# Performance work log

Measured on AMD Instinct MI355X. Metric: run time of the kernel, lower is better.

Reference implementation:

```python
import jax, jax.numpy as jnp
import numpy as np

H = 128          # image_size
FOCAL = 3.0      # camera focal length (NDC scale)
ZNEAR = 1e-2
EPS = 1e-8

def setup_inputs() -> dict:
    key = jax.random.key(0)
    k1, k2, k3, k4 = jax.random.split(key, 4)
    B, V, F = 2, 2048, 512
    verts_world = jax.random.uniform(k1, (B, V, 3), minval=-1.0, maxval=1.0, dtype=jnp.float32)
    faces = jax.random.randint(k2, (F, 3), 0, V)
    R = jnp.tile(jnp.eye(3, dtype=jnp.float32)[None], (B, 1, 1)) + 0.05 * jax.random.normal(k3, (B, 3, 3), dtype=jnp.float32)
    # camera sits 4 units back so all geometry has positive view-space depth
    T = jnp.concatenate([0.1 * jax.random.normal(k4, (B, 2), dtype=jnp.float32), jnp.full((B, 1), 4.0, jnp.float32)], axis=-1)
    return {"verts_world": verts_world, "faces": faces, "R": R, "T": T}

def _seg_d2(px, py, ax, ay, bx, by):
    # squared distance from point (px,py) to segment (a,b)
    abx, aby = bx - ax, by - ay
    apx, apy = px - ax, py - ay
    t = jnp.clip((apx * abx + apy * aby) / (abx * abx + aby * aby + EPS), 0.0, 1.0)
    dx, dy = apx - t * abx, apy - t * aby
    return dx * dx + dy * dy

def _project(verts_world, R, T):
    # world -> view (row-vector convention, as pytorch3d transform_points)
    v_view = jnp.einsum('bvj,bjk->bvk', verts_world, R) + T[:, None, :]
    z = v_view[..., 2:3]                       # view-space depth kept as screen z (as in MeshRasterizer.transform)
    xy = FOCAL * v_view[..., :2] / z           # perspective projection to NDC
    return jnp.concatenate([xy, z], axis=-1)   # [B,V,3]

def _rasterize(verts_ndc, faces):
    tri = verts_ndc[:, faces]                  # [B,F,3,3]
    def c(i, j):
        return tri[:, :, i, j][:, None, None, :]   # [B,1,1,F]
    x0, y0, z0 = c(0, 0), c(0, 1), c(0, 2)
    x1, y1, z1 = c(1, 0), c(1, 1), c(1, 2)
    x2, y2, z2 = c(2, 0), c(2, 1), c(2, 2)
    # pixel centers, pytorch3d NDC convention (+X left, +Y up)
    s = 1.0 - (2.0 * jnp.arange(H, dtype=verts_ndc.dtype) + 1.0) / H
    px = s[None, None, :, None]                # varies over W
    py = s[None, :, None, None]                # varies over H
    area = (x1 - x0) * (y2 - y0) - (y1 - y0) * (x2 - x0)      # 2 * signed area
    denom = jnp.where(jnp.abs(area) > EPS, area, EPS)
    w0 = ((x2 - x1) * (py - y1) - (y2 - y1) * (px - x1)) / denom
    w1 = ((x0 - x2) * (py - y2) - (y0 - y2) * (px - x2)) / denom
    w2 = 1.0 - w0 - w1                         # barycentrics [B,H,W,F]
    inside = (w0 >= 0) & (w1 >= 0) & (w2 >= 0)
    zp = w0 * z0 + w1 * z1 + w2 * z2           # barycentric-interpolated depth
    valid = inside & (zp > ZNEAR) & (jnp.abs(area) > EPS)
    d2 = jnp.minimum(_seg_d2(px, py, x0, y0, x1, y1),
                     jnp.minimum(_seg_d2(px, py, x1, y1, x2, y2),
                                 _seg_d2(px, py, x2, y2, x0, y0)))
    dists = jnp.where(inside, -d2, d2)         # signed squared edge distance
    zsort = jnp.where(valid, zp, jnp.inf)
    idx = jnp.argmin(zsort, axis=-1)           # nearest covering face per pixel (faces_per_pixel=1)
    hit = jnp.isfinite(jnp.min(zsort, axis=-1))
    take = lambda a: jnp.take_along_axis(a, idx[..., None], axis=-1)[..., 0]
    zbuf = jnp.where(hit, take(zp), -1.0)
    bary = jnp.stack([take(w0), take(w1), take(w2)], axis=-1)
    bary = jnp.where(hit[..., None], bary, -1.0)
    dsel = jnp.where(hit, take(dists), -1.0)
    pix_to_face = jnp.where(hit, idx, -1)
    # trailing K=1 (faces_per_pixel) dim, matching Fragments layout
    return pix_to_face[..., None], zbuf[..., None], bary[:, :, :, None, :], dsel[..., None]

def reference(verts_world, faces, R, T):
    verts_ndc = _project(verts_world, R, T)
    return _rasterize(verts_ndc, faces)
```

## Files before the change

kernel.cpp:

```cpp
#include <hip/hip_runtime.h>
#include <cstdint>

#define H_ 128
#define V_ 2048
#define F_ 512
#define B_ 2
#define FOCAL_ 3.0f
#define ZNEAR_ 0.01f
#define EPS_ 1e-8f
#define PAD_ 1e-3f

__global__ __launch_bounds__(1024) void k_prep(const float* __restrict__ vw,
                                               const int* __restrict__ faces,
                                               const float* __restrict__ R,
                                               const float* __restrict__ T,
                                               float* __restrict__ fd,
                                               float4* __restrict__ bb) {
  __shared__ float ndc[B_ * V_ * 3];
  int t = threadIdx.x;

  for (int tid = t; tid < B_ * V_; tid += 1024) {
    int b = tid >> 11;
    const float* v  = vw + tid * 3;
    const float* Rb = R + b * 9;
    const float* Tb = T + b * 3;
    float vx = v[0], vy = v[1], vz = v[2];
    float o[3];
#pragma unroll
    for (int k = 0; k < 3; ++k) {
      float a = __fadd_rn(__fadd_rn(__fmul_rn(vx, Rb[k]), __fmul_rn(vy, Rb[3 + k])),
                          __fmul_rn(vz, Rb[6 + k]));
      o[k] = __fadd_rn(a, Tb[k]);
    }
    float z = o[2];
    ndc[tid * 3 + 0] = __fdiv_rn(__fmul_rn(FOCAL_, o[0]), z);
    ndc[tid * 3 + 1] = __fdiv_rn(__fmul_rn(FOCAL_, o[1]), z);
    ndc[tid * 3 + 2] = z;
  }
  __syncthreads();

  {
    int tid = t;
    int b = tid >> 9;
    int f = tid & (F_ - 1);
    int i0 = faces[f * 3 + 0], i1 = faces[f * 3 + 1], i2 = faces[f * 3 + 2];
    const float* nb = ndc + b * V_ * 3;
    float x0 = nb[i0 * 3], y0 = nb[i0 * 3 + 1], z0 = nb[i0 * 3 + 2];
    float x1 = nb[i1 * 3], y1 = nb[i1 * 3 + 1], z1 = nb[i1 * 3 + 2];
    float x2 = nb[i2 * 3], y2 = nb[i2 * 3 + 1], z2 = nb[i2 * 3 + 2];
    float area = __fsub_rn(__fmul_rn(__fsub_rn(x1, x0), __fsub_rn(y2, y0)),
                           __fmul_rn(__fsub_rn(y1, y0), __fsub_rn(x2, x0)));
    bool ok = fabsf(area) > EPS_;
    float denom = ok ? area : EPS_;
    float* o = fd + tid * 16;
    o[0]  = x1;  o[1]  = y1;  o[2]  = x2;  o[3]  = y2;
    o[4]  = z0;  o[5]  = z1;  o[6]  = z2;  o[7]  = denom;
    o[8]  = __fsub_rn(x2, x1);  o[9]  = __fsub_rn(y2, y1);
    o[10] = __fsub_rn(x0, x2);  o[11] = __fsub_rn(y0, y2);
    o[12] = x0;  o[13] = y0;  o[14] = ok ? 1.0f : 0.0f;  o[15] = 0.0f;
    float4 box;
    if (ok) {
      box.x = fminf(fminf(x0, x1), x2) - PAD_;
      box.y = fmaxf(fmaxf(x0, x1), x2) + PAD_;
      box.z = fminf(fminf(y0, y1), y2) - PAD_;
      box.w = fmaxf(fmaxf(y0, y1), y2) + PAD_;
    } else {
      box.x = 1e30f; box.y = -1e30f; box.z = 1e30f; box.w = -1e30f;
    }
    bb[tid] = box;
  }
}

__device__ __forceinline__ float seg_d2(float px, float py, float ax, float ay,
                                        float bx, float by) {
  float abx = __fsub_rn(bx, ax), aby = __fsub_rn(by, ay);
  float apx = __fsub_rn(px, ax), apy = __fsub_rn(py, ay);
  float num = __fadd_rn(__fmul_rn(apx, abx), __fmul_rn(apy, aby));
  float den = __fadd_rn(__fadd_rn(__fmul_rn(abx, abx), __fmul_rn(aby, aby)), EPS_);
  float t = __fdiv_rn(num, den);
  t = fminf(fmaxf(t, 0.0f), 1.0f);
  float dx = __fsub_rn(apx, __fmul_rn(t, abx));
  float dy = __fsub_rn(apy, __fmul_rn(t, aby));
  return __fadd_rn(__fmul_rn(dx, dx), __fmul_rn(dy, dy));
}

__global__ __launch_bounds__(512) void k_raster(const float* __restrict__ fd,
                                                const float4* __restrict__ bb,
                                                float* __restrict__ out) {
  __shared__ float4 lf4[F_ * 4];
  __shared__ unsigned long long red[64 * 8];
  const float* lf = (const float*)lf4;
  int blk = blockIdx.x;
  int b  = blk >> 8;
  int iy = (blk >> 1) & (H_ - 1);
  int h  = blk & 1;
  int t = threadIdx.x;
  int lane = t & 63;
  int q = t >> 6;
  int ix = h * 64 + lane;

  const float4* src = (const float4*)(fd + b * F_ * 16);
  for (int i = t; i < F_ * 4; i += 512) lf4[i] = src[i];
  __syncthreads();

  float px = 1.0f - (float)(2 * ix + 1) * 0.0078125f;
  float py = 1.0f - (float)(2 * iy + 1) * 0.0078125f;
  float pxmax = 1.0f - (float)(2 * (h * 64) + 1) * 0.0078125f;
  float pxmin = 1.0f - (float)(2 * (h * 64 + 63) + 1) * 0.0078125f;

  float4 box = bb[b * F_ + q * 64 + lane];
  bool ov = (box.x <= pxmax) && (box.y >= pxmin) && (box.z <= py) && (box.w >= py);
  unsigned long long m = __ballot(ov);

  const float INF = __int_as_float(0x7f800000);
  float best = INF;
  int bidx = q * 64;

  while (m) {
    int f = q * 64 + __builtin_ctzll(m);
    m &= m - 1;
    float4 q0 = lf4[f * 4 + 0];
    float4 q1 = lf4[f * 4 + 1];
    float4 q2 = lf4[f * 4 + 2];
    float e0 = __fsub_rn(__fmul_rn(q2.x, __fsub_rn(py, q0.y)),
                         __fmul_rn(q2.y, __fsub_rn(px, q0.x)));
    float e1 = __fsub_rn(__fmul_rn(q2.z, __fsub_rn(py, q0.w)),
                         __fmul_rn(q2.w, __fsub_rn(px, q0.z)));
    bool dpos = q1.w > 0.0f;
    bool s0 = dpos ? (e0 >= 0.0f) : (e0 <= 0.0f);
    bool s1 = dpos ? (e1 >= 0.0f) : (e1 <= 0.0f);
    if (__any(s0 && s1)) {
      float w0 = __fdiv_rn(e0, q1.w);
      float w1 = __fdiv_rn(e1, q1.w);
      float w2 = __fsub_rn(__fsub_rn(1.0f, w0), w1);
      float zp = __fadd_rn(__fadd_rn(__fmul_rn(w0, q1.x), __fmul_rn(w1, q1.y)),
                           __fmul_rn(w2, q1.z));
      bool valid = s0 && s1 && (w2 >= 0.0f) && (zp > ZNEAR_);
      float zs = valid ? zp : INF;
      if (zs < best) { best = zs; bidx = f; }
    }
  }

  red[lane * 8 + q] =
      ((unsigned long long)__float_as_uint(best) << 32) | (unsigned long long)(unsigned)bidx;
  __syncthreads();

  if (q == 0) {
    unsigned long long mm = red[lane * 8];
#pragma unroll
    for (int j = 1; j < 8; ++j) {
      unsigned long long v = red[lane * 8 + j];
      mm = (v < mm) ? v : mm;
    }
    unsigned zb = (unsigned)(mm >> 32);
    int idx = (int)(mm & 0xffffffffu);
    bool hit = zb < 0x7f800000u;

    const float* Fp = &lf[idx * 16];
    float x1 = Fp[0], y1 = Fp[1], x2 = Fp[2], y2 = Fp[3];
    float z0 = Fp[4], z1 = Fp[5], z2 = Fp[6], denom = Fp[7];
    float dx21 = Fp[8], dy21 = Fp[9], dx02 = Fp[10], dy02 = Fp[11];
    float x0 = Fp[12], y0 = Fp[13];
    float w0 = __fdiv_rn(__fsub_rn(__fmul_rn(dx21, __fsub_rn(py, y1)),
                                   __fmul_rn(dy21, __fsub_rn(px, x1))), denom);
    float w1 = __fdiv_rn(__fsub_rn(__fmul_rn(dx02, __fsub_rn(py, y2)),
                                   __fmul_rn(dy02, __fsub_rn(px, x2))), denom);
    float w2 = __fsub_rn(__fsub_rn(1.0f, w0), w1);
    float zp = __fadd_rn(__fadd_rn(__fmul_rn(w0, z0), __fmul_rn(w1, z1)),
                         __fmul_rn(w2, z2));
    float d01 = seg_d2(px, py, x0, y0, x1, y1);
    float d12 = seg_d2(px, py, x1, y1, x2, y2);
    float d20 = seg_d2(px, py, x2, y2, x0, y0);
    float d2 = fminf(d01, fminf(d12, d20));

    int pix = ((b * H_ + iy) * H_) + ix;
    out[pix]                 = hit ? (float)idx : -1.0f;
    out[32768 + pix]         = hit ? zp : -1.0f;
    out[65536 + pix * 3 + 0] = hit ? w0 : -1.0f;
    out[65536 + pix * 3 + 1] = hit ? w1 : -1.0f;
    out[65536 + pix * 3 + 2] = hit ? w2 : -1.0f;
    out[163840 + pix]        = hit ? -d2 : -1.0f;
  }
}

extern "C" void kernel_launch(void* const* d_in, const int* in_sizes, int n_in,
                              void* d_out, int out_size, void* d_ws, size_t ws_size,
                              hipStream_t stream) {
  const float* vw    = (const float*)d_in[0];
  const int*   faces = (const int*)d_in[1];
  const float* R     = (const float*)d_in[2];
  const float* T     = (const float*)d_in[3];
  float* out = (float*)d_out;
  float* ws  = (float*)d_ws;
  float*  fd  = ws;
  float4* bbp = (float4*)(ws + 16384);
  k_prep<<<1, 1024, 0, stream>>>(vw, faces, R, T, fd, bbp);
  k_raster<<<512, 512, 0, stream>>>(fd, bbp, out);
}
```

Before: 84.43 us.

## Fuse projection and face setup into raster kernel, recomputing per block

Removes the single-block prep kernel and its global workspace round trip. Each of the 512 raster blocks now projects all 2048 vertices of its batch and builds the face table and bounding boxes directly in shared memory. This drops one launch and the serial single-block prep stage, at the cost of redundant per-block projection work (divisions included) and about 40 KB of shared memory per block, which may limit occupancy.

```diff
diff --git a/kernel.cpp b/kernel.cpp
--- a/kernel.cpp
+++ b/kernel.cpp
@@ -9,67 +9,6 @@
 #define ZNEAR_ 0.01f
 #define EPS_ 1e-8f
 #define PAD_ 1e-3f
-
-__global__ __launch_bounds__(1024) void k_prep(const float* __restrict__ vw,
-                                               const int* __restrict__ faces,
-                                               const float* __restrict__ R,
-                                               const float* __restrict__ T,
-                                               float* __restrict__ fd,
-                                               float4* __restrict__ bb) {
-  __shared__ float ndc[B_ * V_ * 3];
-  int t = threadIdx.x;
-
-  for (int tid = t; tid < B_ * V_; tid += 1024) {
-    int b = tid >> 11;
-    const float* v  = vw + tid * 3;
-    const float* Rb = R + b * 9;
-    const float* Tb = T + b * 3;
-    float vx = v[0], vy = v[1], vz = v[2];
-    float o[3];
-#pragma unroll
-    for (int k = 0; k < 3; ++k) {
-      float a = __fadd_rn(__fadd_rn(__fmul_rn(vx, Rb[k]), __fmul_rn(vy, Rb[3 + k])),
-                          __fmul_rn(vz, Rb[6 + k]));
-      o[k] = __fadd_rn(a, Tb[k]);
-    }
-    float z = o[2];
-    ndc[tid * 3 + 0] = __fdiv_rn(__fmul_rn(FOCAL_, o[0]), z);
-    ndc[tid * 3 + 1] = __fdiv_rn(__fmul_rn(FOCAL_, o[1]), z);
-    ndc[tid * 3 + 2] = z;
-  }
-  __syncthreads();
-
-  {
-    int tid = t;
-    int b = tid >> 9;
-    int f = tid & (F_ - 1);
-    int i0 = faces[f * 3 + 0], i1 = faces[f * 3 + 1], i2 = faces[f * 3 + 2];
-    const float* nb = ndc + b * V_ * 3;
-    float x0 = nb[i0 * 3], y0 = nb[i0 * 3 + 1], z0 = nb[i0 * 3 + 2];
-    float x1 = nb[i1 * 3], y1 = nb[i1 * 3 + 1], z1 = nb[i1 * 3 + 2];
-    float x2 = nb[i2 * 3], y2 = nb[i2 * 3 + 1], z2 = nb[i2 * 3 + 2];
-    float area = __fsub_rn(__fmul_rn(__fsub_rn(x1, x0), __fsub_rn(y2, y0)),
-                           __fmul_rn(__fsub_rn(y1, y0), __fsub_rn(x2, x0)));
-    bool ok = fabsf(area) > EPS_;
-    float denom = ok ? area : EPS_;
-    float* o = fd + tid * 16;
-    o[0]  = x1;  o[1]  = y1;  o[2]  = x2;  o[3]  = y2;
-    o[4]  = z0;  o[5]  = z1;  o[6]  = z2;  o[7]  = denom;
-    o[8]  = __fsub_rn(x2, x1);  o[9]  = __fsub_rn(y2, y1);
-    o[10] = __fsub_rn(x0, x2);  o[11] = __fsub_rn(y0, y2);
-    o[12] = x0;  o[13] = y0;  o[14] = ok ? 1.0f : 0.0f;  o[15] = 0.0f;
-    float4 box;
-    if (ok) {
-      box.x = fminf(fminf(x0, x1), x2) - PAD_;
-      box.y = fmaxf(fmaxf(x0, x1), x2) + PAD_;
-      box.z = fminf(fminf(y0, y1), y2) - PAD_;
-      box.w = fmaxf(fmaxf(y0, y1), y2) + PAD_;
-    } else {
-      box.x = 1e30f; box.y = -1e30f; box.z = 1e30f; box.w = -1e30f;
-    }
-    bb[tid] = box;
-  }
-}
 
 __device__ __forceinline__ float seg_d2(float px, float py, float ax, float ay,
                                         float bx, float by) {
@@ -84,10 +23,14 @@
   return __fadd_rn(__fmul_rn(dx, dx), __fmul_rn(dy, dy));
 }
 
-__global__ __launch_bounds__(512) void k_raster(const float* __restrict__ fd,
-                                                const float4* __restrict__ bb,
-                                                float* __restrict__ out) {
+__global__ __launch_bounds__(512) void k_all(const float* __restrict__ vw,
+                                             const int* __restrict__ faces,
+                                             const float* __restrict__ R,
+                                             const float* __restrict__ T,
+                                             float* __restrict__ out) {
+  __shared__ float ndc[V_ * 3];
   __shared__ float4 lf4[F_ * 4];
+  __shared__ float4 lbb[F_];
   __shared__ unsigned long long red[64 * 8];
   const float* lf = (const float*)lf4;
   int blk = blockIdx.x;
@@ -99,8 +42,55 @@
   int q = t >> 6;
   int ix = h * 64 + lane;
 
-  const float4* src = (const float4*)(fd + b * F_ * 16);
-  for (int i = t; i < F_ * 4; i += 512) lf4[i] = src[i];
+  {
+    const float* Rb = R + b * 9;
+    const float* Tb = T + b * 3;
+    float r00 = Rb[0], r01 = Rb[1], r02 = Rb[2];
+    float r10 = Rb[3], r11 = Rb[4], r12 = Rb[5];
+    float r20 = Rb[6], r21 = Rb[7], r22 = Rb[8];
+    float t0 = Tb[0], t1 = Tb[1], t2 = Tb[2];
+    for (int i = t; i < V_; i += 512) {
+      const float* v = vw + (b * V_ + i) * 3;
+      float vx = v[0], vy = v[1], vz = v[2];
+      float ox = __fadd_rn(__fadd_rn(__fadd_rn(__fmul_rn(vx, r00), __fmul_rn(vy, r10)),
+                                     __fmul_rn(vz, r20)), t0);
+      float oy = __fadd_rn(__fadd_rn(__fadd_rn(__fmul_rn(vx, r01), __fmul_rn(vy, r11)),
+                                     __fmul_rn(vz, r21)), t1);
+      float oz = __fadd_rn(__fadd_rn(__fadd_rn(__fmul_rn(vx, r02), __fmul_rn(vy, r12)),
+                                     __fmul_rn(vz, r22)), t2);
+      ndc[i * 3 + 0] = __fdiv_rn(__fmul_rn(FOCAL_, ox), oz);
+      ndc[i * 3 + 1] = __fdiv_rn(__fmul_rn(FOCAL_, oy), oz);
+      ndc[i * 3 + 2] = oz;
+    }
+  }
+  __syncthreads();
+
+  {
+    int f = t;
+    int i0 = faces[f * 3 + 0], i1 = faces[f * 3 + 1], i2 = faces[f * 3 + 2];
+    float x0 = ndc[i0 * 3], y0 = ndc[i0 * 3 + 1], z0 = ndc[i0 * 3 + 2];
+    float x1 = ndc[i1 * 3], y1 = ndc[i1 * 3 + 1], z1 = ndc[i1 * 3 + 2];
+    float x2 = ndc[i2 * 3], y2 = ndc[i2 * 3 + 1], z2 = ndc[i2 * 3 + 2];
+    float area = __fsub_rn(__fmul_rn(__fsub_rn(x1, x0), __fsub_rn(y2, y0)),
+                           __fmul_rn(__fsub_rn(y1, y0), __fsub_rn(x2, x0)));
+    bool ok = fabsf(area) > EPS_;
+    float denom = ok ? area : EPS_;
+    lf4[f * 4 + 0] = make_float4(x1, y1, x2, y2);
+    lf4[f * 4 + 1] = make_float4(z0, z1, z2, denom);
+    lf4[f * 4 + 2] = make_float4(__fsub_rn(x2, x1), __fsub_rn(y2, y1),
+                                 __fsub_rn(x0, x2), __fsub_rn(y0, y2));
+    lf4[f * 4 + 3] = make_float4(x0, y0, ok ? 1.0f : 0.0f, 0.0f);
+    float4 box;
+    if (ok) {
+      box.x = fminf(fminf(x0, x1), x2) - PAD_;
+      box.y = fmaxf(fmaxf(x0, x1), x2) + PAD_;
+      box.z = fminf(fminf(y0, y1), y2) - PAD_;
+      box.w = fmaxf(fmaxf(y0, y1), y2) + PAD_;
+    } else {
+      box.x = 1e30f; box.y = -1e30f; box.z = 1e30f; box.w = -1e30f;
+    }
+    lbb[f] = box;
+  }
   __syncthreads();
 
   float px = 1.0f - (float)(2 * ix + 1) * 0.0078125f;
@@ -108,7 +98,7 @@
   float pxmax = 1.0f - (float)(2 * (h * 64) + 1) * 0.0078125f;
   float pxmin = 1.0f - (float)(2 * (h * 64 + 63) + 1) * 0.0078125f;
 
-  float4 box = bb[b * F_ + q * 64 + lane];
+  float4 box = lbb[q * 64 + lane];
   bool ov = (box.x <= pxmax) && (box.y >= pxmin) && (box.z <= py) && (box.w >= py);
   unsigned long long m = __ballot(ov);
 
@@ -191,9 +181,6 @@
   const float* R     = (const float*)d_in[2];
   const float* T     = (const float*)d_in[3];
   float* out = (float*)d_out;
-  float* ws  = (float*)d_ws;
-  float*  fd  = ws;
-  float4* bbp = (float4*)(ws + 16384);
-  k_prep<<<1, 1024, 0, stream>>>(vw, faces, R, T, fd, bbp);
-  k_raster<<<512, 512, 0, stream>>>(fd, bbp, out);
+  (void)d_ws; (void)ws_size;
+  k_all<<<512, 512, 0, stream>>>(vw, faces, R, T, out);
 }
```

Result: faster. 81.39 us (-3.6%).
